# Optimization experiments

Measured on AMD Instinct MI355X. Metric: run time of the kernel, lower is better.

Reference implementation:

```python
import jax, jax.numpy as jnp
import numpy as np

ALPHA = 0.2  # LeakyReLU negative slope


def setup_inputs() -> dict:
    key = jax.random.key(0)
    k1, k2, k3, k4 = jax.random.split(key, 4)
    B, N, F_IN, F_OUT = 4, 4096, 256, 256
    h = jax.random.normal(k1, (B, N, F_IN), dtype=jnp.float32)
    adj = jax.random.randint(k2, (B, N, N), 0, 2, dtype=jnp.int32)
    # xavier_normal with gain=1.414: std = gain*sqrt(2/(fan_in+fan_out))
    std_W = 1.414 * np.sqrt(2.0 / (F_IN + F_OUT))
    W = jax.random.normal(k3, (F_IN, F_OUT), dtype=jnp.float32) * std_W
    std_a = 1.414 * np.sqrt(2.0 / (1 + 2 * F_OUT))
    a = jax.random.normal(k4, (1, 2 * F_OUT), dtype=jnp.float32) * std_a
    return {"h": h, "adj": adj, "W": W, "a": a}


def reference(h, adj, W, a):
    # h: [B, N, F_in], adj: [B, N, N] (0/1), W: [F_in, F_out], a: [1, 2*F_out]
    F_out = W.shape[1]
    Hh = jnp.einsum('bni,io->bno', h, W)               # [B, N, F_out]
    a_src = a[0, :F_out]                                # attends to edge source i
    a_dst = a[0, F_out:]                                # attends to edge target j
    s = jnp.einsum('bno,o->bn', Hh, a_src)              # [B, N]
    d = jnp.einsum('bno,o->bn', Hh, a_dst)              # [B, N]
    # score(i,j) = a . concat(Hh_i, Hh_j) = s_i + d_j
    logits = s[:, :, None] + d[:, None, :]              # [B, N, N]
    # edge_e = exp(-leakyrelu(score)) only on edges (adj nonzero), else 0
    e = jnp.where(adj != 0,
                  jnp.exp(-jax.nn.leaky_relu(logits, negative_slope=ALPHA)),
                  jnp.zeros((), dtype=Hh.dtype))        # [B, N, N]
    rowsum = jnp.sum(e, axis=-1, keepdims=True)         # [B, N, 1]
    # rows with zero sum keep divisor 1 (as in the torch code)
    rowsum = jnp.where(rowsum == 0.0, 1.0, rowsum)
    h_prime = jnp.einsum('bnm,bmo->bno', e, Hh) / rowsum  # [B, N, F_out]
    return jax.nn.elu(h_prime)  # concat=True branch
```

## Files before the change

kernel.cpp:

```cpp
#include <hip/hip_runtime.h>

#define LRELU_ALPHA 0.2f

typedef __bf16 bf16x8 __attribute__((ext_vector_type(8)));
typedef unsigned short u16;
typedef unsigned short u16x8 __attribute__((ext_vector_type(8)));
typedef float f32x4 __attribute__((ext_vector_type(4)));
typedef int int4v __attribute__((ext_vector_type(4)));
typedef unsigned int u32;
typedef unsigned long long u64;

__device__ __forceinline__ u16 f2bf(float f) {
  unsigned int u = __float_as_uint(f);
  u += 0x7fffu + ((u >> 16) & 1u);
  return (u16)(u >> 16);
}

__global__ __launch_bounds__(256) void wcast(const float* __restrict__ W,
                                             u16* __restrict__ WbT) {
  int idx = blockIdx.x * 256 + threadIdx.x;
  WbT[idx] = f2bf(W[(idx & 255) * 256 + (idx >> 8)]);
}

__global__ __launch_bounds__(256) void packgemm(const int* __restrict__ adj,
                                                u32* __restrict__ maskg,
                                                const float* __restrict__ h,
                                                const u16* __restrict__ WbT,
                                                const float* __restrict__ a,
                                                u16* __restrict__ HhTt,
                                                float* __restrict__ sbuf,
                                                float* __restrict__ dbuf) {
  const int tid = threadIdx.x;
  const int l = tid & 63, w = tid >> 6;

  if (blockIdx.x >= 256) {
    const size_t row = (size_t)(blockIdx.x - 256) * 4 + w;
    const int* arow = adj + row * 4096;
    u64* mrow = (u64*)maskg + row * 64;
    for (int ch = 0; ch < 16; ++ch) {
      int4v v = *(const int4v*)(arow + ch * 256 + l * 4);
      u64 b0 = __ballot(v.x != 0);
      u64 b1 = __ballot(v.y != 0);
      u64 b2 = __ballot(v.z != 0);
      u64 b3 = __ballot(v.w != 0);
      if (l == 0) {
        mrow[ch * 4 + 0] = b0;
        mrow[ch * 4 + 1] = b1;
        mrow[ch * 4 + 2] = b2;
        mrow[ch * 4 + 3] = b3;
      }
    }
    return;
  }

  const int bid = blockIdx.x;
  const int lr = l & 15;
  const int lk = (l >> 4) << 3;
  const int rowA = bid * 64 + 16 * w + lr;
  const float* hrow = h + (size_t)rowA * 256 + lk;

  f32x4 acc[16];
#pragma unroll
  for (int n = 0; n < 16; ++n) acc[n] = (f32x4){0.f, 0.f, 0.f, 0.f};

  for (int k0 = 0; k0 < 256; k0 += 32) {
    f32x4 a0 = *(const f32x4*)(hrow + k0);
    f32x4 a1 = *(const f32x4*)(hrow + k0 + 4);
    u16x8 au;
    au[0] = f2bf(a0[0]); au[1] = f2bf(a0[1]); au[2] = f2bf(a0[2]); au[3] = f2bf(a0[3]);
    au[4] = f2bf(a1[0]); au[5] = f2bf(a1[1]); au[6] = f2bf(a1[2]); au[7] = f2bf(a1[3]);
    bf16x8 af = __builtin_bit_cast(bf16x8, au);
#pragma unroll
    for (int n = 0; n < 16; ++n) {
      int4v bv = *(const int4v*)(WbT + (size_t)(16 * n + lr) * 256 + k0 + lk);
      bf16x8 bf = __builtin_bit_cast(bf16x8, bv);
      acc[n] = __builtin_amdgcn_mfma_f32_16x16x32_bf16(af, bf, acc[n], 0, 0, 0);
    }
  }

  float sp[4] = {0.f, 0.f, 0.f, 0.f}, dp[4] = {0.f, 0.f, 0.f, 0.f};
#pragma unroll
  for (int n = 0; n < 16; ++n) {
    int col = 16 * n + lr;
    float as = a[col];
    float ad = a[256 + col];
#pragma unroll
    for (int rr = 0; rr < 4; ++rr) {
      int row = bid * 64 + 16 * w + ((l >> 4) << 2) + rr;
      int bb = row >> 12, kk = row & 4095;
      float v = acc[n][rr];
      size_t addr = (size_t)bb * 1048576 + (size_t)(kk >> 5) * 8192 +
                    (col >> 4) * 512 + ((kk >> 3) & 3) * 128 + (col & 15) * 8 +
                    (kk & 7);
      HhTt[addr] = f2bf(v);
      sp[rr] += v * as;
      dp[rr] += v * ad;
    }
  }
#pragma unroll
  for (int rr = 0; rr < 4; ++rr) {
#pragma unroll
    for (int off = 1; off < 16; off <<= 1) {
      sp[rr] += __shfl_xor(sp[rr], off);
      dp[rr] += __shfl_xor(dp[rr], off);
    }
  }
  if ((l & 15) == 0) {
#pragma unroll
    for (int rr = 0; rr < 4; ++rr) {
      int row = bid * 64 + 16 * w + ((l >> 4) << 2) + rr;
      sbuf[row] = sp[rr];
      dbuf[row] = dp[rr];
    }
  }
}

__global__ __launch_bounds__(1024, 4) void gat_main(const u32* __restrict__ maskg,
                                                    const u16* __restrict__ HhTt,
                                                    const float* __restrict__ s,
                                                    const float* __restrict__ d,
                                                    float* __restrict__ out) {
  __shared__ __align__(16) u32 Mk[64 * 131];
  __shared__ __align__(16) u16 At[4][2560];
  __shared__ float rs_lds[64];

  const int tid = threadIdx.x, bid = blockIdx.x;
  const int xcd = bid & 7;
  const int t = (xcd << 5) | (bid >> 3);
  const int b = t >> 6;
  const int rowbase = (t & 63) << 6;

  const int l = tid & 63, w = tid >> 6;
  const int lr = l & 15, lkg = l >> 4;
  const int r = tid >> 4, kp = tid & 15;

  {
    const u32* mrow = maskg + ((size_t)(b * 4096 + rowbase)) * 128;
#pragma unroll
    for (int j = 0; j < 8; ++j)
      Mk[r * 131 + kp * 8 + j] = mrow[r * 128 + kp * 8 + j];
  }
  const float s_r = s[b * 4096 + rowbase + r];
  const float* dtp = d + b * 4096 + kp * 2;
  const int mkr = r * 131;

  float racc = 0.f;

#define EGEN(BUF, STE)                                                        \
  {                                                                           \
    const int wb_ = ((STE) >> 3) * 8 + (kp & 1) * 4 + (((STE) & 7) >> 2);     \
    const int bp_ = ((STE) & 3) * 8 + (kp >> 1);                              \
    u32 w0_ = Mk[mkr + wb_];                                                  \
    u32 w1_ = Mk[mkr + wb_ + 2];                                              \
    float2 dv = *(const float2*)(dtp + (STE) * 32);                           \
    float lg0 = s_r + dv.x;                                                   \
    float t0 = fmaxf(lg0, LRELU_ALPHA * lg0);                                 \
    float e0 = ((w0_ >> bp_) & 1u) ? __expf(-t0) : 0.f;                       \
    float lg1 = s_r + dv.y;                                                   \
    float t1 = fmaxf(lg1, LRELU_ALPHA * lg1);                                 \
    float e1 = ((w1_ >> bp_) & 1u) ? __expf(-t1) : 0.f;                       \
    racc += e0 + e1;                                                          \
    u32 pk;                                                                   \
    asm("v_cvt_pk_bf16_f32 %0, %1, %2" : "=v"(pk) : "v"(e0), "v"(e1));        \
    *(u32*)&At[BUF][r * 40 + kp * 2] = pk;                                    \
  }

  __syncthreads();
  EGEN(0, 0)

  const char* bbase = (const char*)HhTt + (size_t)b * 2097152 + w * 1024 + l * 16;
  int4v Bcur = *(const int4v*)(bbase);

  f32x4 acc[4];
#pragma unroll
  for (int n = 0; n < 4; ++n) acc[n] = (f32x4){0.f, 0.f, 0.f, 0.f};

  for (int st = 0; st < 128; ++st) {
    if (st < 127) EGEN((st + 1) & 3, st + 1)
    const int pst = (st < 127) ? st + 1 : st;
    int4v Bnext = *(const int4v*)(bbase + (size_t)pst * 16384);

    asm volatile("s_waitcnt lgkmcnt(0)" ::: "memory");
    __builtin_amdgcn_s_barrier();
    __builtin_amdgcn_sched_barrier(0);

    const u16* atb = &At[st & 3][0];
    int4v a0 = *(const int4v*)(atb + (0 * 16 + lr) * 40 + lkg * 8);
    int4v a1 = *(const int4v*)(atb + (1 * 16 + lr) * 40 + lkg * 8);
    int4v a2 = *(const int4v*)(atb + (2 * 16 + lr) * 40 + lkg * 8);
    int4v a3 = *(const int4v*)(atb + (3 * 16 + lr) * 40 + lkg * 8);
    bf16x8 bfv = __builtin_bit_cast(bf16x8, Bcur);
    __builtin_amdgcn_s_setprio(1);
    acc[0] = __builtin_amdgcn_mfma_f32_16x16x32_bf16(
        __builtin_bit_cast(bf16x8, a0), bfv, acc[0], 0, 0, 0);
    acc[1] = __builtin_amdgcn_mfma_f32_16x16x32_bf16(
        __builtin_bit_cast(bf16x8, a1), bfv, acc[1], 0, 0, 0);
    acc[2] = __builtin_amdgcn_mfma_f32_16x16x32_bf16(
        __builtin_bit_cast(bf16x8, a2), bfv, acc[2], 0, 0, 0);
    acc[3] = __builtin_amdgcn_mfma_f32_16x16x32_bf16(
        __builtin_bit_cast(bf16x8, a3), bfv, acc[3], 0, 0, 0);
    __builtin_amdgcn_s_setprio(0);
    Bcur = Bnext;
  }
#undef EGEN

  racc += __shfl_xor(racc, 1);
  racc += __shfl_xor(racc, 2);
  racc += __shfl_xor(racc, 4);
  racc += __shfl_xor(racc, 8);
  if (kp == 0) rs_lds[r] = (racc == 0.f) ? 1.f : racc;
  __syncthreads();

#pragma unroll
  for (int rt = 0; rt < 4; ++rt) {
#pragma unroll
    for (int reg = 0; reg < 4; ++reg) {
      int rloc = rt * 16 + lkg * 4 + reg;
      float rsv = rs_lds[rloc];
      float v = acc[rt][reg] / rsv;
      out[((size_t)(b * 4096 + rowbase + rloc)) * 256 + w * 16 + lr] =
          v > 0.f ? v : (__expf(v) - 1.f);
    }
  }
}

extern "C" void kernel_launch(void* const* d_in, const int* in_sizes, int n_in,
                              void* d_out, int out_size, void* d_ws, size_t ws_size,
                              hipStream_t stream) {
  const float* h = (const float*)d_in[0];
  const int* adj = (const int*)d_in[1];
  const float* W = (const float*)d_in[2];
  const float* a = (const float*)d_in[3];
  float* out = (float*)d_out;

  u16* WbT   = (u16*)d_ws;
  u16* HhTt  = (u16*)((char*)d_ws + 131072);
  float* sb  = (float*)((char*)d_ws + 131072 + 8388608);
  float* db  = sb + 16384;
  u32* maskg = (u32*)((char*)d_ws + 131072 + 8388608 + 131072);

  hipLaunchKernelGGL(wcast,    dim3(256),  dim3(256),  0, stream, W, WbT);
  hipLaunchKernelGGL(packgemm, dim3(4352), dim3(256),  0, stream,
                     adj, maskg, h, WbT, a, HhTt, sb, db);
  hipLaunchKernelGGL(gat_main, dim3(256),  dim3(1024), 0, stream,
                     maskg, HhTt, sb, db, out);
}
```

Measured before the change: 181.0 us.

## Fuse mask packing, projection GEMM and attention into one cooperative kernel

Merges the packgemm and gat_main kernels into a single cooperative launch. Each block packs the adjacency bits for its own 64 rows straight into shared memory instead of going through a global mask buffer. The first four waves then compute the projected features and the s/d scores, and a grid-wide sync separates that phase from the attention phase. This removes a kernel launch and the global mask round trip. In exchange, the adjacency read and the GEMM now run on only 256 blocks, where they previously had 4352 smaller blocks for parallelism, and a grid barrier is added.

```diff
diff --git a/kernel.cpp b/kernel.cpp
--- a/kernel.cpp
+++ b/kernel.cpp
@@ -1,4 +1,7 @@
 #include <hip/hip_runtime.h>
+#include <hip/hip_cooperative_groups.h>
+
+namespace cg = cooperative_groups;
 
 #define LRELU_ALPHA 0.2f
 
@@ -22,21 +25,33 @@
   WbT[idx] = f2bf(W[(idx & 255) * 256 + (idx >> 8)]);
 }
 
-__global__ __launch_bounds__(256) void packgemm(const int* __restrict__ adj,
-                                                u32* __restrict__ maskg,
-                                                const float* __restrict__ h,
-                                                const u16* __restrict__ WbT,
-                                                const float* __restrict__ a,
-                                                u16* __restrict__ HhTt,
-                                                float* __restrict__ sbuf,
-                                                float* __restrict__ dbuf) {
-  const int tid = threadIdx.x;
+__global__ __launch_bounds__(1024, 4) void fused(const int* __restrict__ adj,
+                                                 const float* __restrict__ h,
+                                                 const u16* __restrict__ WbT,
+                                                 const float* __restrict__ a,
+                                                 u16* __restrict__ HhTt,
+                                                 float* __restrict__ sbuf,
+                                                 float* __restrict__ dbuf,
+                                                 float* __restrict__ out) {
+  __shared__ __align__(16) u32 Mk[64 * 131];
+  __shared__ __align__(16) u16 At[4][2560];
+  __shared__ float rs_lds[64];
+
+  cg::grid_group grid = cg::this_grid();
+
+  const int tid = threadIdx.x, bid = blockIdx.x;
+  const int xcd = bid & 7;
+  const int t = (xcd << 5) | (bid >> 3);
+  const int b = t >> 6;
+  const int rowbase = (t & 63) << 6;
+  const size_t growbase = (size_t)b * 4096 + rowbase;
+
   const int l = tid & 63, w = tid >> 6;
 
-  if (blockIdx.x >= 256) {
-    const size_t row = (size_t)(blockIdx.x - 256) * 4 + w;
-    const int* arow = adj + row * 4096;
-    u64* mrow = (u64*)maskg + row * 64;
+#pragma unroll
+  for (int q = 0; q < 4; ++q) {
+    const int r = w * 4 + q;
+    const int* arow = adj + (growbase + r) * 4096;
     for (int ch = 0; ch < 16; ++ch) {
       int4v v = *(const int4v*)(arow + ch * 256 + l * 4);
       u64 b0 = __ballot(v.x != 0);
@@ -44,104 +59,85 @@
       u64 b2 = __ballot(v.z != 0);
       u64 b3 = __ballot(v.w != 0);
       if (l == 0) {
-        mrow[ch * 4 + 0] = b0;
-        mrow[ch * 4 + 1] = b1;
-        mrow[ch * 4 + 2] = b2;
-        mrow[ch * 4 + 3] = b3;
-      }
-    }
-    return;
-  }
-
-  const int bid = blockIdx.x;
-  const int lr = l & 15;
-  const int lk = (l >> 4) << 3;
-  const int rowA = bid * 64 + 16 * w + lr;
-  const float* hrow = h + (size_t)rowA * 256 + lk;
-
-  f32x4 acc[16];
-#pragma unroll
-  for (int n = 0; n < 16; ++n) acc[n] = (f32x4){0.f, 0.f, 0.f, 0.f};
-
-  for (int k0 = 0; k0 < 256; k0 += 32) {
-    f32x4 a0 = *(const f32x4*)(hrow + k0);
-    f32x4 a1 = *(const f32x4*)(hrow + k0 + 4);
-    u16x8 au;
-    au[0] = f2bf(a0[0]); au[1] = f2bf(a0[1]); au[2] = f2bf(a0[2]); au[3] = f2bf(a0[3]);
-    au[4] = f2bf(a1[0]); au[5] = f2bf(a1[1]); au[6] = f2bf(a1[2]); au[7] = f2bf(a1[3]);
-    bf16x8 af = __builtin_bit_cast(bf16x8, au);
+        const int base = r * 131 + ch * 8;
+        Mk[base + 0] = (u32)b0; Mk[base + 1] = (u32)(b0 >> 32);
+        Mk[base + 2] = (u32)b1; Mk[base + 3] = (u32)(b1 >> 32);
+        Mk[base + 4] = (u32)b2; Mk[base + 5] = (u32)(b2 >> 32);
+        Mk[base + 6] = (u32)b3; Mk[base + 7] = (u32)(b3 >> 32);
+      }
+    }
+  }
+
+  if (tid < 256) {
+    const int w4 = tid >> 6;
+    const int lr4 = l & 15;
+    const int lk = (l >> 4) << 3;
+    const size_t rowA = growbase + 16 * w4 + lr4;
+    const float* hrow = h + rowA * 256 + lk;
+
+    f32x4 acc[16];
+#pragma unroll
+    for (int n = 0; n < 16; ++n) acc[n] = (f32x4){0.f, 0.f, 0.f, 0.f};
+
+    for (int k0 = 0; k0 < 256; k0 += 32) {
+      f32x4 a0 = *(const f32x4*)(hrow + k0);
+      f32x4 a1 = *(const f32x4*)(hrow + k0 + 4);
+      u16x8 au;
+      au[0] = f2bf(a0[0]); au[1] = f2bf(a0[1]); au[2] = f2bf(a0[2]); au[3] = f2bf(a0[3]);
+      au[4] = f2bf(a1[0]); au[5] = f2bf(a1[1]); au[6] = f2bf(a1[2]); au[7] = f2bf(a1[3]);
+      bf16x8 af = __builtin_bit_cast(bf16x8, au);
+#pragma unroll
+      for (int n = 0; n < 16; ++n) {
+        int4v bv = *(const int4v*)(WbT + (size_t)(16 * n + lr4) * 256 + k0 + lk);
+        bf16x8 bf = __builtin_bit_cast(bf16x8, bv);
+        acc[n] = __builtin_amdgcn_mfma_f32_16x16x32_bf16(af, bf, acc[n], 0, 0, 0);
+      }
+    }
+
+    float sp[4] = {0.f, 0.f, 0.f, 0.f}, dp[4] = {0.f, 0.f, 0.f, 0.f};
 #pragma unroll
     for (int n = 0; n < 16; ++n) {
-      int4v bv = *(const int4v*)(WbT + (size_t)(16 * n + lr) * 256 + k0 + lk);
-      bf16x8 bf = __builtin_bit_cast(bf16x8, bv);
-      acc[n] = __builtin_amdgcn_mfma_f32_16x16x32_bf16(af, bf, acc[n], 0, 0, 0);
-    }
-  }
-
-  float sp[4] = {0.f, 0.f, 0.f, 0.f}, dp[4] = {0.f, 0.f, 0.f, 0.f};
-#pragma unroll
-  for (int n = 0; n < 16; ++n) {
-    int col = 16 * n + lr;
-    float as = a[col];
-    float ad = a[256 + col];
+      int col = 16 * n + lr4;
+      float as = a[col];
+      float ad = a[256 + col];
+#pragma unroll
+      for (int rr = 0; rr < 4; ++rr) {
+        size_t row = growbase + 16 * w4 + ((l >> 4) << 2) + rr;
+        int bb = (int)(row >> 12), kk = (int)(row & 4095);
+        float v = acc[n][rr];
+        size_t addr = (size_t)bb * 1048576 + (size_t)(kk >> 5) * 8192 +
+                      (col >> 4) * 512 + ((kk >> 3) & 3) * 128 + (col & 15) * 8 +
+                      (kk & 7);
+        HhTt[addr] = f2bf(v);
+        sp[rr] += v * as;
+        dp[rr] += v * ad;
+      }
+    }
 #pragma unroll
     for (int rr = 0; rr < 4; ++rr) {
-      int row = bid * 64 + 16 * w + ((l >> 4) << 2) + rr;
-      int bb = row >> 12, kk = row & 4095;
-      float v = acc[n][rr];
-      size_t addr = (size_t)bb * 1048576 + (size_t)(kk >> 5) * 8192 +
-                    (col >> 4) * 512 + ((kk >> 3) & 3) * 128 + (col & 15) * 8 +
-                    (kk & 7);
-      HhTt[addr] = f2bf(v);
-      sp[rr] += v * as;
-      dp[rr] += v * ad;
-    }
-  }
-#pragma unroll
-  for (int rr = 0; rr < 4; ++rr) {
-#pragma unroll
-    for (int off = 1; off < 16; off <<= 1) {
-      sp[rr] += __shfl_xor(sp[rr], off);
-      dp[rr] += __shfl_xor(dp[rr], off);
-    }
-  }
-  if ((l & 15) == 0) {
-#pragma unroll
-    for (int rr = 0; rr < 4; ++rr) {
-      int row = bid * 64 + 16 * w + ((l >> 4) << 2) + rr;
-      sbuf[row] = sp[rr];
-      dbuf[row] = dp[rr];
-    }
-  }
-}
-
-__global__ __launch_bounds__(1024, 4) void gat_main(const u32* __restrict__ maskg,
-                                                    const u16* __restrict__ HhTt,
-                                                    const float* __restrict__ s,
-                                                    const float* __restrict__ d,
-                                                    float* __restrict__ out) {
-  __shared__ __align__(16) u32 Mk[64 * 131];
-  __shared__ __align__(16) u16 At[4][2560];
-  __shared__ float rs_lds[64];
-
-  const int tid = threadIdx.x, bid = blockIdx.x;
-  const int xcd = bid & 7;
-  const int t = (xcd << 5) | (bid >> 3);
-  const int b = t >> 6;
-  const int rowbase = (t & 63) << 6;
-
-  const int l = tid & 63, w = tid >> 6;
+#pragma unroll
+      for (int off = 1; off < 16; off <<= 1) {
+        sp[rr] += __shfl_xor(sp[rr], off);
+        dp[rr] += __shfl_xor(dp[rr], off);
+      }
+    }
+    if ((l & 15) == 0) {
+#pragma unroll
+      for (int rr = 0; rr < 4; ++rr) {
+        size_t row = growbase + 16 * w4 + ((l >> 4) << 2) + rr;
+        sbuf[row] = sp[rr];
+        dbuf[row] = dp[rr];
+      }
+    }
+  }
+
+  grid.sync();
+
   const int lr = l & 15, lkg = l >> 4;
   const int r = tid >> 4, kp = tid & 15;
 
-  {
-    const u32* mrow = maskg + ((size_t)(b * 4096 + rowbase)) * 128;
-#pragma unroll
-    for (int j = 0; j < 8; ++j)
-      Mk[r * 131 + kp * 8 + j] = mrow[r * 128 + kp * 8 + j];
-  }
-  const float s_r = s[b * 4096 + rowbase + r];
-  const float* dtp = d + b * 4096 + kp * 2;
+  const float s_r = sbuf[growbase + r];
+  const float* dtp = dbuf + (size_t)b * 4096 + kp * 2;
   const int mkr = r * 131;
 
   float racc = 0.f;
@@ -165,7 +161,6 @@
     *(u32*)&At[BUF][r * 40 + kp * 2] = pk;                                    \
   }
 
-  __syncthreads();
   EGEN(0, 0)
 
   const char* bbase = (const char*)HhTt + (size_t)b * 2097152 + w * 1024 + l * 16;
@@ -218,7 +213,7 @@
       int rloc = rt * 16 + lkg * 4 + reg;
       float rsv = rs_lds[rloc];
       float v = acc[rt][reg] / rsv;
-      out[((size_t)(b * 4096 + rowbase + rloc)) * 256 + w * 16 + lr] =
+      out[(growbase + rloc) * 256 + w * 16 + lr] =
           v > 0.f ? v : (__expf(v) - 1.f);
     }
   }
@@ -227,21 +222,21 @@
 extern "C" void kernel_launch(void* const* d_in, const int* in_sizes, int n_in,
                               void* d_out, int out_size, void* d_ws, size_t ws_size,
                               hipStream_t stream) {
+  const int* adj = (const int*)d_in[1];
   const float* h = (const float*)d_in[0];
-  const int* adj = (const int*)d_in[1];
   const float* W = (const float*)d_in[2];
   const float* a = (const float*)d_in[3];
   float* out = (float*)d_out;
 
-  u16* WbT   = (u16*)d_ws;
-  u16* HhTt  = (u16*)((char*)d_ws + 131072);
-  float* sb  = (float*)((char*)d_ws + 131072 + 8388608);
-  float* db  = sb + 16384;
-  u32* maskg = (u32*)((char*)d_ws + 131072 + 8388608 + 131072);
-
-  hipLaunchKernelGGL(wcast,    dim3(256),  dim3(256),  0, stream, W, WbT);
-  hipLaunchKernelGGL(packgemm, dim3(4352), dim3(256),  0, stream,
-                     adj, maskg, h, WbT, a, HhTt, sb, db);
-  hipLaunchKernelGGL(gat_main, dim3(256),  dim3(1024), 0, stream,
-                     maskg, HhTt, sb, db, out);
-}
+  u16* WbT  = (u16*)d_ws;
+  u16* HhTt = (u16*)((char*)d_ws + 131072);
+  float* sb = (float*)((char*)d_ws + 131072 + 8388608);
+  float* db = sb + 16384;
+
+  hipLaunchKernelGGL(wcast, dim3(256), dim3(256), 0, stream, W, WbT);
+
+  void* args[] = {(void*)&adj, (void*)&h, (void*)&WbT, (void*)&a,
+                  (void*)&HhTt, (void*)&sb, (void*)&db, (void*)&out};
+  hipLaunchCooperativeKernel((void*)fused, dim3(256), dim3(1024), args, 0,
+                             stream);
+}
```

Result: slower. 204.1 us (+12.8%).
